# Optimization experiments

Hardware: AMD Instinct MI355X
Metric: run time of the kernel (lower is better)

## Reference

```python
import jax, jax.numpy as jnp
import numpy as np

B, SQ, SK, D, H = 8, 1024, 1024, 768, 12
HD = D // H  # 64


def setup_inputs() -> dict:
    key = jax.random.key(0)
    ks = jax.random.split(key, 6)
    s = 0.02
    return {
        "hidden_states": jax.random.normal(ks[0], (B, SQ, D), jnp.float32),
        "context": jax.random.normal(ks[1], (B, SK, D), jnp.float32),
        "attention_mask": jnp.zeros((B, 1, 1, SK), jnp.float32),
        "Wq": jax.random.normal(ks[2], (D, D), jnp.float32) * s,
        "bq": jnp.zeros((D,), jnp.float32),
        "Wk": jax.random.normal(ks[3], (D, D), jnp.float32) * s,
        "bk": jnp.zeros((D,), jnp.float32),
        "Wv": jax.random.normal(ks[4], (D, D), jnp.float32) * s,
        "bv": jnp.zeros((D,), jnp.float32),
    }


def _split_heads(x):
    # [B, S, D] -> [B, H, S, HD]
    b, s, _ = x.shape
    return x.reshape(b, s, H, HD).transpose(0, 2, 1, 3)


def reference(hidden_states, context, attention_mask, Wq, bq, Wk, bk, Wv, bv):
    q = _split_heads(hidden_states @ Wq + bq)   # [B,H,SQ,HD]
    k = _split_heads(context @ Wk + bk)         # [B,H,SK,HD]
    v = _split_heads(context @ Wv + bv)         # [B,H,SK,HD]
    scores = jnp.einsum("bhqd,bhkd->bhqk", q, k) / jnp.sqrt(jnp.float32(HD))
    scores = scores + attention_mask            # broadcast [B,1,1,SK]
    probs = jax.nn.softmax(scores, axis=-1)     # dropout p=0 -> identity
    ctx = jnp.einsum("bhqk,bhkd->bhqd", probs, v)
    return ctx.transpose(0, 2, 1, 3).reshape(hidden_states.shape[0], -1, H * HD)
```

## Files before the change

kernel.cpp:

```cpp
#include <hip/hip_runtime.h>
#include <hip/hip_bf16.h>
#include <cstdint>

#define B_  8
#define SQ_ 1024
#define SK_ 1024
#define D_  768
#define H_  12
#define HD_ 64

typedef __attribute__((ext_vector_type(8))) short s16x8;
typedef __attribute__((ext_vector_type(4))) float f32x4;
typedef __attribute__((ext_vector_type(16))) float f32x16;

__device__ __forceinline__ float bf2f(ushort u) {
    union { uint32_t i; float f; } v; v.i = ((uint32_t)u) << 16; return v.f;
}
__device__ __forceinline__ ushort f2bf(float f) {
    __hip_bfloat16 h = __float2bfloat16(f);
    union { __hip_bfloat16 h; ushort u; } v; v.h = h; return v.u;
}
__device__ __forceinline__ uint32_t pk32(float a, float b) {
    return (uint32_t)f2bf(a) | ((uint32_t)f2bf(b) << 16);
}
__device__ __forceinline__ float fexp2(float x) {
#if __has_builtin(__builtin_amdgcn_exp2f)
    return __builtin_amdgcn_exp2f(x);
#else
    return exp2f(x);
#endif
}
__device__ __forceinline__ void xch(uint32_t a, uint32_t b, bool lo, uint32_t& x, uint32_t& y) {
    uint32_t bx = (uint32_t)__shfl_xor((int)b, 32);
    uint32_t ax = (uint32_t)__shfl_xor((int)a, 32);
    x = lo ? a : bx;
    y = lo ? ax : b;
}

__global__ void convX(const float4* __restrict__ src, ushort* __restrict__ dst, int n4) {
    int i = blockIdx.x * blockDim.x + threadIdx.x;
    int stride = gridDim.x * blockDim.x;
    for (; i < n4; i += stride) {
        float4 v = src[i];
        ushort4 o = { f2bf(v.x), f2bf(v.y), f2bf(v.z), f2bf(v.w) };
        *reinterpret_cast<ushort4*>(dst + (size_t)i * 4) = o;
    }
}

__global__ void convWT(const float* __restrict__ W, ushort* __restrict__ WT) {
    __shared__ float t[32][33];
    int k0 = blockIdx.x * 32, n0 = blockIdx.y * 32;
    int tx = threadIdx.x & 31, ty = threadIdx.x >> 5;
#pragma unroll
    for (int rr = 0; rr < 4; ++rr)
        t[ty + 8 * rr][tx] = W[(size_t)(k0 + ty + 8 * rr) * D_ + n0 + tx];
    __syncthreads();
#pragma unroll
    for (int rr = 0; rr < 4; ++rr)
        WT[(size_t)(n0 + ty + 8 * rr) * D_ + k0 + tx] = f2bf(t[tx][ty + 8 * rr]);
}

#define GL16(g, l)                                                                     \
    __builtin_amdgcn_global_load_lds((const __attribute__((address_space(1))) void*)(g), \
                                     (__attribute__((address_space(3))) void*)(l), 16, 0, 0)

__global__ __launch_bounds__(256) void gemm_qkv(
    const ushort* __restrict__ hb, const ushort* __restrict__ cb,
    const ushort* __restrict__ wqt, const ushort* __restrict__ wkt, const ushort* __restrict__ wvt,
    const float* __restrict__ bq, const float* __restrict__ bk, const float* __restrict__ bv,
    ushort* __restrict__ qout, ushort* __restrict__ kout, ushort* __restrict__ vtout)
{
    const int z = blockIdx.z;
    const ushort* A    = (z == 0) ? hb : cb;
    const ushort* Wt   = (z == 0) ? wqt : (z == 1) ? wkt : wvt;
    const float*  bias = (z == 0) ? bq  : (z == 1) ? bk  : bv;

    __shared__ ushort As[128 * 32];
    __shared__ ushort Bs[128 * 32];

    const int tid = threadIdx.x;
    const int w = tid >> 6, l = tid & 63;
    const int g = l >> 4, c = l & 15;
    const int wr = w >> 1, wc = w & 1;
    const int m0 = blockIdx.x * 128;
    const int n0 = blockIdx.y * 128;

    f32x4 acc[4][4];
#pragma unroll
    for (int mi = 0; mi < 4; ++mi)
#pragma unroll
        for (int ni = 0; ni < 4; ++ni) acc[mi][ni] = (f32x4){0.f, 0.f, 0.f, 0.f};

    for (int kt = 0; kt < D_ / 32; ++kt) {
        __syncthreads();
#pragma unroll
        for (int j = 0; j < 2; ++j) {
            int cc = (j * 4 + w) * 64 + l;
            int row = cc >> 2, c8 = cc & 3;
            const ushort* ga = A  + (size_t)(m0 + row) * D_ + kt * 32 + c8 * 8;
            GL16(ga, (char*)As + (size_t)(j * 4 + w) * 1024);
            const ushort* gb = Wt + (size_t)(n0 + row) * D_ + kt * 32 + c8 * 8;
            GL16(gb, (char*)Bs + (size_t)(j * 4 + w) * 1024);
        }
        __syncthreads();

        s16x8 af[4], bfr[4];
#pragma unroll
        for (int mi = 0; mi < 4; ++mi)
            af[mi] = *(const s16x8*)&As[(wr * 64 + mi * 16 + c) * 32 + g * 8];
#pragma unroll
        for (int ni = 0; ni < 4; ++ni)
            bfr[ni] = *(const s16x8*)&Bs[(wc * 64 + ni * 16 + c) * 32 + g * 8];
#pragma unroll
        for (int mi = 0; mi < 4; ++mi)
#pragma unroll
            for (int ni = 0; ni < 4; ++ni)
                acc[mi][ni] = __builtin_amdgcn_mfma_f32_16x16x32_bf16(af[mi], bfr[ni], acc[mi][ni], 0, 0, 0);
    }

    if (z < 2) {
        ushort* Out = (z == 0) ? qout : kout;
#pragma unroll
        for (int ni = 0; ni < 4; ++ni) {
            int ncol = n0 + wc * 64 + ni * 16 + c;
            float bv_ = bias[ncol];
#pragma unroll
            for (int mi = 0; mi < 4; ++mi) {
#pragma unroll
                for (int r = 0; r < 4; ++r) {
                    int mrow = m0 + wr * 64 + mi * 16 + 4 * g + r;
                    Out[(size_t)mrow * D_ + ncol] = f2bf(acc[mi][ni][r] + bv_);
                }
            }
        }
    } else {
#pragma unroll
        for (int ni = 0; ni < 4; ++ni) {
            int ncol = n0 + wc * 64 + ni * 16 + c;
            float bv_ = bias[ncol];
            int hh = ncol >> 6, dd = ncol & 63;
#pragma unroll
            for (int mi = 0; mi < 4; ++mi) {
                int mrow = m0 + wr * 64 + mi * 16 + 4 * g;
                int bb = mrow >> 10, ss = mrow & 1023;
                ushort4 pk;
                pk.x = f2bf(acc[mi][ni][0] + bv_);
                pk.y = f2bf(acc[mi][ni][1] + bv_);
                pk.z = f2bf(acc[mi][ni][2] + bv_);
                pk.w = f2bf(acc[mi][ni][3] + bv_);
                *reinterpret_cast<ushort4*>(vtout + (size_t)((bb * H_ + hh) * HD_ + dd) * SK_ + ss) = pk;
            }
        }
    }
}

#define MFMA32(a, b, c) __builtin_amdgcn_mfma_f32_32x32x16_bf16(a, b, c, 0, 0, 0)

__device__ __forceinline__ void proc_qs(f32x16 sa, float& m_run, float& ps,
                                        f32x16& o0, f32x16& o1,
                                        const s16x8 v0a, const s16x8 v1a,
                                        const s16x8 v0b, const s16x8 v1b,
                                        const int hi, const bool lo)
{
    const float L2E = 1.44269504f;
    float a0 = fmaxf(fmaxf(sa[0], sa[1]), fmaxf(sa[2], sa[3]));
    float a1 = fmaxf(fmaxf(sa[4], sa[5]), fmaxf(sa[6], sa[7]));
    float a2 = fmaxf(fmaxf(sa[8], sa[9]), fmaxf(sa[10], sa[11]));
    float a3 = fmaxf(fmaxf(sa[12], sa[13]), fmaxf(sa[14], sa[15]));
    float pmax = fmaxf(fmaxf(a0, a1), fmaxf(a2, a3));
    if (__any(pmax > m_run + 8.f)) {
        float mf = fmaxf(pmax, __shfl_xor(pmax, 32));
        float mn = fmaxf(m_run, mf);
        float alpha = fexp2((m_run - mn) * L2E);
        m_run = mn; ps *= alpha;
#pragma unroll
        for (int r = 0; r < 16; ++r) {
            float ar = __shfl(alpha, (r & 3) + 8 * (r >> 2) + 4 * hi);
            o0[r] *= ar; o1[r] *= ar;
        }
    }
    float ml = m_run * L2E;
    float p[16];
#pragma unroll
    for (int r = 0; r < 16; ++r) p[r] = fexp2(sa[r] * L2E - ml);
    ps += (((p[0] + p[1]) + (p[2] + p[3])) + ((p[4] + p[5]) + (p[6] + p[7]))) +
          (((p[8] + p[9]) + (p[10] + p[11])) + ((p[12] + p[13]) + (p[14] + p[15])));
    uint32_t cc[8];
#pragma unroll
    for (int j = 0; j < 8; ++j) cc[j] = pk32(p[2 * j], p[2 * j + 1]);
    uint32_t d0, d1, d2, d3, e0, e1, e2, e3;
    xch(cc[0], cc[2], lo, d0, d2);
    xch(cc[1], cc[3], lo, d1, d3);
    xch(cc[4], cc[6], lo, e0, e2);
    xch(cc[5], cc[7], lo, e1, e3);
    union { uint32_t u[4]; s16x8 v; } ua, ub;
    ua.u[0] = d0; ua.u[1] = d1; ua.u[2] = d2; ua.u[3] = d3;
    ub.u[0] = e0; ub.u[1] = e1; ub.u[2] = e2; ub.u[3] = e3;
    o0 = MFMA32(ua.v, v0a, o0);
    o0 = MFMA32(ub.v, v1a, o0);
    o1 = MFMA32(ua.v, v0b, o1);
    o1 = MFMA32(ub.v, v1b, o1);
}

__global__ __launch_bounds__(128, 2) void attn(
    const ushort* __restrict__ Qb, const ushort* __restrict__ Kb, const ushort* __restrict__ VT,
    const float* __restrict__ amask, float* __restrict__ out)
{
    __shared__ ushort Ks[2][64 * 64];
    __shared__ ushort Vs[2][64 * 64];
    __shared__ float  Ms[1024];

    const int tid = threadIdx.x;
    const int w   = tid >> 6;
    const int l   = tid & 63;
    const int hi  = l >> 5;
    const int l31 = l & 31;
    const bool lo = (hi == 0);
    const int swz = (l31 & 7) << 4;
    const int q0  = blockIdx.x * 128 + w * 64;
    const int h = blockIdx.y, b = blockIdx.z;

    ((float4*)Ms)[tid]       = ((const float4*)(amask + b * SK_))[tid];
    ((float4*)Ms)[tid + 128] = ((const float4*)(amask + b * SK_))[tid + 128];

    s16x8 qf[2][4];
#pragma unroll
    for (int qs = 0; qs < 2; ++qs)
#pragma unroll
        for (int s = 0; s < 4; ++s) {
            const ushort* gq = Qb + (size_t)(b * SQ_ + q0 + qs * 32 + l31) * D_ + h * HD_ + s * 16 + hi * 8;
            s16x8 v = *(const s16x8*)gq;
#pragma unroll
            for (int i = 0; i < 8; ++i) v[i] = (short)f2bf(bf2f((ushort)v[i]) * 0.125f);
            qf[qs][s] = v;
        }

    const int row0 = tid >> 3, c8 = tid & 7;
    const int ldsoff = row0 * 128 + ((c8 * 16) ^ ((row0 & 7) << 4));
    const ushort* kp = Kb + (size_t)(b * SK_ + row0) * D_ + h * HD_ + c8 * 8;
    const ushort* vp = VT + (size_t)((b * H_ + h) * HD_ + row0) * SK_ + c8 * 8;

    {
#pragma unroll
        for (int i = 0; i < 4; ++i) {
            *(uint4*)((char*)Ks[0] + ldsoff + 2048 * i) = *(const uint4*)(kp + i * 16 * D_);
            *(uint4*)((char*)Vs[0] + ldsoff + 2048 * i) = *(const uint4*)(vp + i * 16 * SK_);
        }
        kp += 64 * D_; vp += 64;
    }
    __syncthreads();

    f32x16 o[2][2];
#pragma unroll
    for (int qs = 0; qs < 2; ++qs)
#pragma unroll
        for (int db = 0; db < 2; ++db)
#pragma unroll
            for (int r = 0; r < 16; ++r) o[qs][db][r] = 0.f;
    float m_run[2] = { -INFINITY, -INFINITY };
    float ps[2] = { 0.f, 0.f };

#define TILE(CUR, NXT, T)                                                              \
    {                                                                                  \
        uint4 nk0 = *(const uint4*)(kp);                                               \
        uint4 nk1 = *(const uint4*)(kp + 16 * D_);                                     \
        uint4 nk2 = *(const uint4*)(kp + 32 * D_);                                     \
        uint4 nk3 = *(const uint4*)(kp + 48 * D_);                                     \
        uint4 nv0 = *(const uint4*)(vp);                                               \
        uint4 nv1 = *(const uint4*)(vp + 16 * SK_);                                    \
        uint4 nv2 = *(const uint4*)(vp + 32 * SK_);                                    \
        uint4 nv3 = *(const uint4*)(vp + 48 * SK_);                                    \
        if ((T) < 14) { kp += 64 * D_; vp += 64; }                                     \
        _Pragma("unroll")                                                              \
        for (int blk = 0; blk < 2; ++blk) {                                            \
            const int kvb = (T) * 64 + blk * 32;                                       \
            union { f32x4 q[4]; f32x16 v; } mku;                                       \
            _Pragma("unroll")                                                          \
            for (int t = 0; t < 4; ++t)                                                \
                mku.q[t] = *(const f32x4*)&Ms[kvb + 4 * hi + 8 * t];                   \
            s16x8 kfr[4];                                                              \
            _Pragma("unroll")                                                          \
            for (int s = 0; s < 4; ++s)                                                \
                kfr[s] = *(const s16x8*)((const char*)Ks[CUR] + (blk * 32 + l31) * 128 \
                                         + ((s * 32 + hi * 16) ^ swz));                \
            s16x8 vfr[2][2];                                                           \
            _Pragma("unroll")                                                          \
            for (int sl = 0; sl < 2; ++sl)                                             \
                _Pragma("unroll")                                                      \
                for (int db = 0; db < 2; ++db)                                         \
                    vfr[sl][db] = *(const s16x8*)((const char*)Vs[CUR] +               \
                        (db * 32 + l31) * 128 + ((blk * 64 + sl * 32 + hi * 16) ^ swz)); \
            _Pragma("unroll")                                                          \
            for (int qs = 0; qs < 2; ++qs) {                                           \
                f32x16 sa = MFMA32(kfr[0], qf[qs][0], mku.v);                          \
                sa = MFMA32(kfr[1], qf[qs][1], sa);                                    \
                sa = MFMA32(kfr[2], qf[qs][2], sa);                                    \
                sa = MFMA32(kfr[3], qf[qs][3], sa);                                    \
                proc_qs(sa, m_run[qs], ps[qs], o[qs][0], o[qs][1],                     \
                        vfr[0][0], vfr[1][0], vfr[0][1], vfr[1][1], hi, lo);           \
            }                                                                          \
        }                                                                              \
        *(uint4*)((char*)Ks[NXT] + ldsoff)        = nk0;                               \
        *(uint4*)((char*)Ks[NXT] + ldsoff + 2048) = nk1;                               \
        *(uint4*)((char*)Ks[NXT] + ldsoff + 4096) = nk2;                               \
        *(uint4*)((char*)Ks[NXT] + ldsoff + 6144) = nk3;                               \
        *(uint4*)((char*)Vs[NXT] + ldsoff)        = nv0;                               \
        *(uint4*)((char*)Vs[NXT] + ldsoff + 2048) = nv1;                               \
        *(uint4*)((char*)Vs[NXT] + ldsoff + 4096) = nv2;                               \
        *(uint4*)((char*)Vs[NXT] + ldsoff + 6144) = nv3;                               \
        __syncthreads();                                                               \
    }

    for (int tt = 0; tt < 8; ++tt) {
        TILE(0, 1, 2 * tt)
        TILE(1, 0, 2 * tt + 1)
    }
#undef TILE

#pragma unroll
    for (int qs = 0; qs < 2; ++qs) {
        float pf = ps[qs] + __shfl_xor(ps[qs], 32);
        float inv = 1.f / pf;
#pragma unroll
        for (int r = 0; r < 16; ++r) {
            int qr = (r & 3) + 8 * (r >> 2) + 4 * hi;
            float iv = __shfl(inv, qr);
            float* op = out + (size_t)(b * SQ_ + q0 + qs * 32 + qr) * D_ + h * HD_ + l31;
            op[0]  = o[qs][0][r] * iv;
            op[32] = o[qs][1][r] * iv;
        }
    }
}

extern "C" void kernel_launch(void* const* d_in, const int* in_sizes, int n_in,
                              void* d_out, int out_size, void* d_ws, size_t ws_size,
                              hipStream_t stream) {
    (void)in_sizes; (void)n_in; (void)out_size; (void)ws_size;
    const float* hidden  = (const float*)d_in[0];
    const float* context = (const float*)d_in[1];
    const float* amask   = (const float*)d_in[2];
    const float* Wq = (const float*)d_in[3];
    const float* bq = (const float*)d_in[4];
    const float* Wk = (const float*)d_in[5];
    const float* bk = (const float*)d_in[6];
    const float* Wv = (const float*)d_in[7];
    const float* bv = (const float*)d_in[8];
    float* out = (float*)d_out;

    char* ws = (char*)d_ws;
    ushort* hb  = (ushort*)(ws);
    ushort* cb  = (ushort*)(ws + 12582912);
    ushort* wqt = (ushort*)(ws + 25165824);
    ushort* wkt = (ushort*)(ws + 26345472);
    ushort* wvt = (ushort*)(ws + 27525120);
    ushort* qb  = (ushort*)(ws + 28704768);
    ushort* kb  = (ushort*)(ws + 41287680);
    ushort* vt  = (ushort*)(ws + 53870592);

    int n4 = (B_ * SQ_ * D_) / 4;
    convX<<<2048, 256, 0, stream>>>((const float4*)hidden, hb, n4);
    convX<<<2048, 256, 0, stream>>>((const float4*)context, cb, n4);
    dim3 gw(24, 24);
    convWT<<<gw, 256, 0, stream>>>(Wq, wqt);
    convWT<<<gw, 256, 0, stream>>>(Wk, wkt);
    convWT<<<gw, 256, 0, stream>>>(Wv, wvt);
    gemm_qkv<<<dim3(64, 6, 3), 256, 0, stream>>>(hb, cb, wqt, wkt, wvt, bq, bk, bv, qb, kb, vt);
    attn<<<dim3(8, 12, 8), 128, 0, stream>>>(qb, kb, vt, amask, out);
}
```

Measured before the change: 234.7 us.

## Split attention block into four waves of 32 query rows each

The attention kernel now launches 256 threads per block instead of 128. Each wave handles 32 query rows instead of 64, so it keeps half as many accumulator and Q-fragment registers, and the launch bounds now allow three blocks per CU. Each thread loads half as many K/V rows into shared memory per tile, since there are twice as many threads to share the load. In exchange, every K/V fragment read from LDS is reused across fewer MFMAs per wave, LDS read traffic per unit of work doubles, and each barrier has to synchronise more waves.

Result: faster. 218.7 us (-6.8%).

```diff
diff --git a/kernel.cpp b/kernel.cpp
--- a/kernel.cpp
+++ b/kernel.cpp
@@ -202,7 +202,7 @@
     o1 = MFMA32(ub.v, v1b, o1);
 }
 
-__global__ __launch_bounds__(128, 2) void attn(
+__global__ __launch_bounds__(256, 3) void attn(
     const ushort* __restrict__ Qb, const ushort* __restrict__ Kb, const ushort* __restrict__ VT,
     const float* __restrict__ amask, float* __restrict__ out)
 {
@@ -217,23 +217,20 @@
     const int l31 = l & 31;
     const bool lo = (hi == 0);
     const int swz = (l31 & 7) << 4;
-    const int q0  = blockIdx.x * 128 + w * 64;
+    const int q0w = blockIdx.x * 128 + w * 32;
     const int h = blockIdx.y, b = blockIdx.z;
 
-    ((float4*)Ms)[tid]       = ((const float4*)(amask + b * SK_))[tid];
-    ((float4*)Ms)[tid + 128] = ((const float4*)(amask + b * SK_))[tid + 128];
-
-    s16x8 qf[2][4];
-#pragma unroll
-    for (int qs = 0; qs < 2; ++qs)
-#pragma unroll
-        for (int s = 0; s < 4; ++s) {
-            const ushort* gq = Qb + (size_t)(b * SQ_ + q0 + qs * 32 + l31) * D_ + h * HD_ + s * 16 + hi * 8;
-            s16x8 v = *(const s16x8*)gq;
-#pragma unroll
-            for (int i = 0; i < 8; ++i) v[i] = (short)f2bf(bf2f((ushort)v[i]) * 0.125f);
-            qf[qs][s] = v;
-        }
+    ((float4*)Ms)[tid] = ((const float4*)(amask + b * SK_))[tid];
+
+    s16x8 qf[4];
+#pragma unroll
+    for (int s = 0; s < 4; ++s) {
+        const ushort* gq = Qb + (size_t)(b * SQ_ + q0w + l31) * D_ + h * HD_ + s * 16 + hi * 8;
+        s16x8 v = *(const s16x8*)gq;
+#pragma unroll
+        for (int i = 0; i < 8; ++i) v[i] = (short)f2bf(bf2f((ushort)v[i]) * 0.125f);
+        qf[s] = v;
+    }
 
     const int row0 = tid >> 3, c8 = tid & 7;
     const int ldsoff = row0 * 128 + ((c8 * 16) ^ ((row0 & 7) << 4));
@@ -241,35 +238,27 @@
     const ushort* vp = VT + (size_t)((b * H_ + h) * HD_ + row0) * SK_ + c8 * 8;
 
     {
-#pragma unroll
-        for (int i = 0; i < 4; ++i) {
-            *(uint4*)((char*)Ks[0] + ldsoff + 2048 * i) = *(const uint4*)(kp + i * 16 * D_);
-            *(uint4*)((char*)Vs[0] + ldsoff + 2048 * i) = *(const uint4*)(vp + i * 16 * SK_);
-        }
+        *(uint4*)((char*)Ks[0] + ldsoff)        = *(const uint4*)(kp);
+        *(uint4*)((char*)Ks[0] + ldsoff + 4096) = *(const uint4*)(kp + 32 * D_);
+        *(uint4*)((char*)Vs[0] + ldsoff)        = *(const uint4*)(vp);
+        *(uint4*)((char*)Vs[0] + ldsoff + 4096) = *(const uint4*)(vp + 32 * SK_);
         kp += 64 * D_; vp += 64;
     }
     __syncthreads();
 
-    f32x16 o[2][2];
-#pragma unroll
-    for (int qs = 0; qs < 2; ++qs)
-#pragma unroll
-        for (int db = 0; db < 2; ++db)
-#pragma unroll
-            for (int r = 0; r < 16; ++r) o[qs][db][r] = 0.f;
-    float m_run[2] = { -INFINITY, -INFINITY };
-    float ps[2] = { 0.f, 0.f };
+    f32x16 o[2];
+#pragma unroll
+    for (int db = 0; db < 2; ++db)
+#pragma unroll
+        for (int r = 0; r < 16; ++r) o[db][r] = 0.f;
+    float m_run = -INFINITY, ps = 0.f;
 
 #define TILE(CUR, NXT, T)                                                              \
     {                                                                                  \
         uint4 nk0 = *(const uint4*)(kp);                                               \
-        uint4 nk1 = *(const uint4*)(kp + 16 * D_);                                     \
-        uint4 nk2 = *(const uint4*)(kp + 32 * D_);                                     \
-        uint4 nk3 = *(const uint4*)(kp + 48 * D_);                                     \
+        uint4 nk1 = *(const uint4*)(kp + 32 * D_);                                     \
         uint4 nv0 = *(const uint4*)(vp);                                               \
-        uint4 nv1 = *(const uint4*)(vp + 16 * SK_);                                    \
-        uint4 nv2 = *(const uint4*)(vp + 32 * SK_);                                    \
-        uint4 nv3 = *(const uint4*)(vp + 48 * SK_);                                    \
+        uint4 nv1 = *(const uint4*)(vp + 32 * SK_);                                    \
         if ((T) < 14) { kp += 64 * D_; vp += 64; }                                     \
         _Pragma("unroll")                                                              \
         for (int blk = 0; blk < 2; ++blk) {                                            \
@@ -290,24 +279,17 @@
                 for (int db = 0; db < 2; ++db)                                         \
                     vfr[sl][db] = *(const s16x8*)((const char*)Vs[CUR] +               \
                         (db * 32 + l31) * 128 + ((blk * 64 + sl * 32 + hi * 16) ^ swz)); \
-            _Pragma("unroll")                                                          \
-            for (int qs = 0; qs < 2; ++qs) {                                           \
-                f32x16 sa = MFMA32(kfr[0], qf[qs][0], mku.v);                          \
-                sa = MFMA32(kfr[1], qf[qs][1], sa);                                    \
-                sa = MFMA32(kfr[2], qf[qs][2], sa);                                    \
-                sa = MFMA32(kfr[3], qf[qs][3], sa);                                    \
-                proc_qs(sa, m_run[qs], ps[qs], o[qs][0], o[qs][1],                     \
-                        vfr[0][0], vfr[1][0], vfr[0][1], vfr[1][1], hi, lo);           \
-            }                                                                          \
+            f32x16 sa = MFMA32(kfr[0], qf[0], mku.v);                                  \
+            sa = MFMA32(kfr[1], qf[1], sa);                                            \
+            sa = MFMA32(kfr[2], qf[2], sa);                                            \
+            sa = MFMA32(kfr[3], qf[3], sa);                                            \
+            proc_qs(sa, m_run, ps, o[0], o[1],                                         \
+                    vfr[0][0], vfr[1][0], vfr[0][1], vfr[1][1], hi, lo);               \
         }                                                                              \
         *(uint4*)((char*)Ks[NXT] + ldsoff)        = nk0;                               \
-        *(uint4*)((char*)Ks[NXT] + ldsoff + 2048) = nk1;                               \
-        *(uint4*)((char*)Ks[NXT] + ldsoff + 4096) = nk2;                               \
-        *(uint4*)((char*)Ks[NXT] + ldsoff + 6144) = nk3;                               \
+        *(uint4*)((char*)Ks[NXT] + ldsoff + 4096) = nk1;                               \
         *(uint4*)((char*)Vs[NXT] + ldsoff)        = nv0;                               \
-        *(uint4*)((char*)Vs[NXT] + ldsoff + 2048) = nv1;                               \
-        *(uint4*)((char*)Vs[NXT] + ldsoff + 4096) = nv2;                               \
-        *(uint4*)((char*)Vs[NXT] + ldsoff + 6144) = nv3;                               \
+        *(uint4*)((char*)Vs[NXT] + ldsoff + 4096) = nv1;                               \
         __syncthreads();                                                               \
     }
 
@@ -317,18 +299,15 @@
     }
 #undef TILE
 
-#pragma unroll
-    for (int qs = 0; qs < 2; ++qs) {
-        float pf = ps[qs] + __shfl_xor(ps[qs], 32);
-        float inv = 1.f / pf;
-#pragma unroll
-        for (int r = 0; r < 16; ++r) {
-            int qr = (r & 3) + 8 * (r >> 2) + 4 * hi;
-            float iv = __shfl(inv, qr);
-            float* op = out + (size_t)(b * SQ_ + q0 + qs * 32 + qr) * D_ + h * HD_ + l31;
-            op[0]  = o[qs][0][r] * iv;
-            op[32] = o[qs][1][r] * iv;
-        }
+    float pf = ps + __shfl_xor(ps, 32);
+    float inv = 1.f / pf;
+#pragma unroll
+    for (int r = 0; r < 16; ++r) {
+        int qr = (r & 3) + 8 * (r >> 2) + 4 * hi;
+        float iv = __shfl(inv, qr);
+        float* op = out + (size_t)(b * SQ_ + q0w + qr) * D_ + h * HD_ + l31;
+        op[0]  = o[0][r] * iv;
+        op[32] = o[1][r] * iv;
     }
 }
 
@@ -365,5 +344,5 @@
     convWT<<<gw, 256, 0, stream>>>(Wk, wkt);
     convWT<<<gw, 256, 0, stream>>>(Wv, wvt);
     gemm_qkv<<<dim3(64, 6, 3), 256, 0, stream>>>(hb, cb, wqt, wkt, wvt, bq, bk, bv, qb, kb, vt);
-    attn<<<dim3(8, 12, 8), 128, 0, stream>>>(qb, kb, vt, amask, out);
-}
+    attn<<<dim3(8, 12, 8), 256, 0, stream>>>(qb, kb, vt, amask, out);
+}
```
